# Performance work log

Measured on AMD Instinct MI355X. Metric: run time of the kernel, lower is better.

Reference implementation:

```python
import jax, jax.numpy as jnp
import numpy as np

NUM_Q_HEADS = 32
NUM_KV_HEADS = 8
HEAD_DIM = 128
ROPE_THETA = 10000.0
Q_SIZE = NUM_Q_HEADS * HEAD_DIM      # 4096
KV_SIZE = NUM_KV_HEADS * HEAD_DIM    # 1024


def _apply_rope_neox(x, positions, theta=ROPE_THETA):
    # x: [T, H, D]; neox-style rotate-halves RoPE
    T, H, D = x.shape
    half = D // 2
    inv_freq = 1.0 / (theta ** (jnp.arange(half, dtype=jnp.float32) / half))
    freqs = positions.astype(jnp.float32)[:, None] * inv_freq[None, :]  # [T, half]
    cos = jnp.cos(freqs)[:, None, :]  # [T, 1, half]
    sin = jnp.sin(freqs)[:, None, :]
    x1, x2 = x[..., :half], x[..., half:]
    return jnp.concatenate([x1 * cos - x2 * sin, x2 * cos + x1 * sin], axis=-1).astype(x.dtype)


def setup_inputs() -> dict:
    key = jax.random.key(0)
    k1, k2, k3 = jax.random.split(key, 3)
    T, E = 8192, 4096
    hidden_states = jax.random.normal(k1, (T, E), dtype=jnp.float32) * 0.02
    positions = jnp.arange(T, dtype=jnp.int32)
    w_qkv = jax.random.normal(k2, (E, Q_SIZE + 2 * KV_SIZE), dtype=jnp.float32) * 0.02
    w_o = jax.random.normal(k3, (Q_SIZE, E), dtype=jnp.float32) * 0.02
    return {"hidden_states": hidden_states, "positions": positions, "w_qkv": w_qkv, "w_o": w_o}


def reference(hidden_states, positions, w_qkv, w_o):
    T = hidden_states.shape[0]
    qkv = hidden_states @ w_qkv                              # [T, 6144]
    q = qkv[:, :Q_SIZE].reshape(T, NUM_Q_HEADS, HEAD_DIM)
    k = qkv[:, Q_SIZE:Q_SIZE + KV_SIZE].reshape(T, NUM_KV_HEADS, HEAD_DIM)
    v = qkv[:, Q_SIZE + KV_SIZE:]                            # [T, KV_SIZE] (unused by stub)
    q = _apply_rope_neox(q, positions)
    k = _apply_rope_neox(k, positions)
    # Attention is stubbed in the source (randn_like(q)); we use the RoPE'd q
    # as the deterministic stand-in so the pipeline stays reproducible.
    attn_output = q.reshape(T, Q_SIZE)
    output = attn_output @ w_o                               # [T, 4096]
    return output
```

## Files before the change

### kernel.cpp

```cpp
#include <hip/hip_runtime.h>
#include <hip/hip_bf16.h>
#include <stdint.h>

#define T_DIM 8192
#define E_DIM 4096
#define NQH   32
#define HD    128
#define QSZ   (NQH * HD)
#define QKV_COLS 6144

typedef unsigned short u16;
typedef __attribute__((ext_vector_type(8))) short   bf16x8;
typedef __attribute__((ext_vector_type(4))) float   f32x4;
typedef __attribute__((ext_vector_type(4))) unsigned short u16x4;

__device__ __forceinline__ u16 f2bf(float f) {
    uint32_t u = __float_as_uint(f);
    u += 0x7fffu + ((u >> 16) & 1u);
    return (u16)(u >> 16);
}
__device__ __forceinline__ float bf2f(u16 u) {
    return __uint_as_float(((uint32_t)u) << 16);
}

__device__ __forceinline__ void gload_lds16(u16* lds, const u16* g) {
    __builtin_amdgcn_global_load_lds(
        (const __attribute__((address_space(1))) uint32_t*)g,
        (__attribute__((address_space(3))) uint32_t*)lds,
        16, 0, 0);
}

__global__ void convert_f32_bf16(const float* __restrict__ in, u16* __restrict__ out, size_t n4) {
    size_t i = (size_t)blockIdx.x * blockDim.x + threadIdx.x;
    size_t stride = (size_t)gridDim.x * blockDim.x;
    for (; i < n4; i += stride) {
        float4 v = ((const float4*)in)[i];
        u16x4 o;
        o.x = f2bf(v.x); o.y = f2bf(v.y); o.z = f2bf(v.z); o.w = f2bf(v.w);
        ((u16x4*)out)[i] = o;
    }
}

__global__ void transpose_conv(const float* __restrict__ W, u16* __restrict__ Wt,
                               int K, int N, int ldW, int colOff) {
    __shared__ float tile[32][33];
    const int tx = threadIdx.x, ty = threadIdx.y;
    const int n0 = blockIdx.x * 32, k0 = blockIdx.y * 32;
#pragma unroll
    for (int j = 0; j < 4; ++j) {
        int k = k0 + ty + j * 8;
        tile[ty + j * 8][tx] = W[(size_t)k * ldW + colOff + n0 + tx];
    }
    __syncthreads();
#pragma unroll
    for (int j = 0; j < 4; ++j) {
        int n = n0 + ty + j * 8;
        Wt[(size_t)n * K + k0 + tx] = f2bf(tile[tx][ty + j * 8]);
    }
}

__global__ void rope_table(const int* __restrict__ pos, float2* __restrict__ tab) {
    int idx = blockIdx.x * blockDim.x + threadIdx.x;
    int t = idx >> 6, d = idx & 63;
    float inv = powf(10000.0f, -(float)d * (1.0f / 64.0f));
    float fr  = (float)pos[t] * inv;
    float s, c;
    sincosf(fr, &s, &c);
    tab[idx] = make_float2(c, s);
}

__device__ __forceinline__ void store_out(u16* p, float v)  { *p = f2bf(v); }
__device__ __forceinline__ void store_out(float* p, float v){ *p = v; }

#define BARS()    do { __builtin_amdgcn_sched_barrier(0); __builtin_amdgcn_s_barrier(); } while (0)
#define BARSPUB() do { __builtin_amdgcn_sched_barrier(0); __builtin_amdgcn_s_barrier(); \
                       __builtin_amdgcn_sched_barrier(0); } while (0)
#define VMC(N) asm volatile("s_waitcnt vmcnt(%0)" :: "n"(N) : "memory")

#define STG_A(buf, h, kOff) do { \
    const u16* s_ = sA + (size_t)(h) * 128 * K + (kOff); \
    u16* d_ = dL + (buf) * 32768 + (h) * 8192; \
    gload_lds16(d_, s_); gload_lds16(d_ + 4096, s_ + (size_t)64 * K); } while (0)
#define STG_B(buf, h, kOff) do { \
    const u16* s_ = sB + (size_t)(h) * 128 * K + (kOff); \
    u16* d_ = dL + 16384 + (buf) * 32768 + (h) * 8192; \
    gload_lds16(d_, s_); gload_lds16(d_ + 4096, s_ + (size_t)64 * K); } while (0)

#define RD_A(buf, miBase, d0, d1) do { _Pragma("unroll") \
    for (int m = 0; m < 4; ++m) { \
        const u16* p_ = lds + (buf) * 32768 + wm * 8192 + ((miBase) + m) * 1024 + aRow; \
        d0[m] = *(const bf16x8*)(p_ + cOf0); \
        d1[m] = *(const bf16x8*)(p_ + cOf1); } } while (0)
#define RD_B(buf, niBase, d0, d1) do { _Pragma("unroll") \
    for (int n = 0; n < 2; ++n) { \
        const int ni_ = (niBase) + n; \
        const u16* p_ = lds + (buf) * 32768 + 16384 + (ni_ >> 1) * 8192 + \
                        ((ni_ & 1) * 64 + wn * 16) * 64 + aRow; \
        d0[n] = *(const bf16x8*)(p_ + cOf0); \
        d1[n] = *(const bf16x8*)(p_ + cOf1); } } while (0)

#define MM(miBase, niBase, A0, A1, B0, B1) do { \
    __builtin_amdgcn_s_setprio(1); \
    _Pragma("unroll") for (int m = 0; m < 4; ++m) \
    _Pragma("unroll") for (int n = 0; n < 2; ++n) { \
        acc[(miBase) + m][(niBase) + n] = __builtin_amdgcn_mfma_f32_16x16x32_bf16( \
            A0[m], B0[n], acc[(miBase) + m][(niBase) + n], 0, 0, 0); \
        acc[(miBase) + m][(niBase) + n] = __builtin_amdgcn_mfma_f32_16x16x32_bf16( \
            A1[m], B1[n], acc[(miBase) + m][(niBase) + n], 0, 0, 0); } \
    __builtin_amdgcn_s_setprio(0); } while (0)

template <typename OutT, bool ROPE>
__global__ __launch_bounds__(512, 2) void gemm256(const u16* __restrict__ A,
                                                  const u16* __restrict__ Bt,
                                                  OutT* __restrict__ C,
                                                  const float2* __restrict__ tab,
                                                  int M, int N, int K) {
    __shared__ u16 lds[65536];
    const int tid  = threadIdx.x;
    const int lane = tid & 63;
    const int wid  = tid >> 6;
    const int wm = wid >> 2;
    const int wn = wid & 3;
    const int lr  = lane & 15;
    const int kq  = lane >> 4;
    const int lr7 = lr & 7;
    const int aRow = lr * 64;
    const int cOf0 = ((kq) ^ lr7) << 3;
    const int cOf1 = ((4 + kq) ^ lr7) << 3;

    const int nwg = gridDim.x;
    const int cpx = nwg >> 3;
    const int bid = blockIdx.x;
    const int swz = (bid & 7) * cpx + (bid >> 3);
    const int numM = M >> 8;
    const size_t rowBase = (size_t)(swz % numM) << 8;
    const size_t colBase = (size_t)(swz / numM) << 8;

    const int r0 = tid >> 3;
    const int cS = (((tid & 7) ^ (r0 & 7)) << 3);
    const u16* sA = A  + (rowBase + r0) * (size_t)K + cS;
    const u16* sB = Bt + (colBase + r0) * (size_t)K + cS;
    u16* dL = &lds[0] + tid * 8;

    f32x4 acc[8][4];
#pragma unroll
    for (int i = 0; i < 8; ++i)
#pragma unroll
        for (int j = 0; j < 4; ++j)
            acc[i][j] = (f32x4){0.f, 0.f, 0.f, 0.f};

    bf16x8 a0K0[4], a0K1[4], a4K0[4], a4K1[4];
    bf16x8 b01eK0[2], b01eK1[2], b01oK0[2], b01oK1[2], b23K0[2], b23K1[2];

    STG_A(0, 0, 0); STG_A(0, 1, 0); STG_B(0, 0, 0); STG_B(0, 1, 0);
    STG_B(1, 0, 64); STG_B(1, 1, 64);
    VMC(4);
    BARSPUB();
    RD_A(0, 0, a0K0, a0K1);
    RD_B(0, 0, b01eK0, b01eK1);

    const int nIter = K >> 7;
    for (int it = 0; it < nIter; ++it) {
        const int k1  = ((it << 1) + 1) << 6;
        const int kt2 = ((it << 1) + 2) << 6;
        const int kt3 = ((it << 1) + 3) << 6;
        const int k2c = (kt2 <= K - 64) ? kt2 : 0;
        const int k3c = (kt3 <= K - 64) ? kt3 : 0;

        STG_A(1, 0, k1);
        BARS();
        RD_B(0, 2, b23K0, b23K1);
        MM(0, 0, a0K0, a0K1, b01eK0, b01eK1);
        STG_A(1, 1, k1);
        BARS();
        RD_A(0, 4, a4K0, a4K1);
        MM(0, 2, a0K0, a0K1, b23K0, b23K1);
        STG_B(0, 0, k2c);
        BARS();
        MM(4, 2, a4K0, a4K1, b23K0, b23K1);
        STG_B(0, 1, k2c);
        VMC(4);
        BARSPUB();
        RD_A(1, 0, a0K0, a0K1);
        RD_B(1, 0, b01oK0, b01oK1);
        MM(4, 0, a4K0, a4K1, b01eK0, b01eK1);
        STG_A(0, 0, k2c);
        BARS();
        RD_B(1, 2, b23K0, b23K1);
        MM(0, 0, a0K0, a0K1, b01oK0, b01oK1);
        STG_A(0, 1, k2c);
        BARS();
        RD_A(1, 4, a4K0, a4K1);
        MM(0, 2, a0K0, a0K1, b23K0, b23K1);
        STG_B(1, 0, k3c);
        BARS();
        MM(4, 2, a4K0, a4K1, b23K0, b23K1);
        STG_B(1, 1, k3c);
        VMC(4);
        BARSPUB();
        RD_A(0, 0, a0K0, a0K1);
        RD_B(0, 0, b01eK0, b01eK1);
        MM(4, 0, a4K0, a4K1, b01oK0, b01oK1);
    }

    asm volatile("s_waitcnt vmcnt(0)" ::: "memory");

    if constexpr (ROPE) {
        const int dIdx = wn * 16 + lr;
#pragma unroll
        for (int mi = 0; mi < 8; ++mi)
#pragma unroll
            for (int r = 0; r < 4; ++r) {
                size_t row = rowBase + wm * 128 + mi * 16 + (kq << 2) + r;
                float2 cs = tab[row * 64 + dIdx];
#pragma unroll
                for (int hp = 0; hp < 2; ++hp) {
                    float x1 = acc[mi][hp * 2 + 0][r];
                    float x2 = acc[mi][hp * 2 + 1][r];
                    size_t c1 = colBase + hp * 128 + wn * 16 + lr;
                    C[row * (size_t)N + c1]      = f2bf(x1 * cs.x - x2 * cs.y);
                    C[row * (size_t)N + c1 + 64] = f2bf(x2 * cs.x + x1 * cs.y);
                }
            }
    } else {
#pragma unroll
        for (int mi = 0; mi < 8; ++mi)
#pragma unroll
            for (int ni = 0; ni < 4; ++ni)
#pragma unroll
                for (int r = 0; r < 4; ++r) {
                    size_t row = rowBase + wm * 128 + mi * 16 + (kq << 2) + r;
                    size_t col = colBase + ni * 64 + wn * 16 + lr;
                    store_out(&C[row * (size_t)N + col], acc[mi][ni][r]);
                }
    }
}

extern "C" void kernel_launch(void* const* d_in, const int* in_sizes, int n_in,
                              void* d_out, int out_size, void* d_ws, size_t ws_size,
                              hipStream_t stream) {
    const float* hidden    = (const float*)d_in[0];
    const int*   positions = (const int*)d_in[1];
    const float* w_qkv     = (const float*)d_in[2];
    const float* w_o       = (const float*)d_in[3];
    float* out = (float*)d_out;

    u16* Hb  = (u16*)d_ws;
    u16* WqT = Hb  + (size_t)T_DIM * E_DIM;
    u16* WoT = WqT + (size_t)QSZ * E_DIM;
    u16* Qb  = WoT + (size_t)E_DIM * QSZ;
    float2* tab = (float2*)WoT;

    convert_f32_bf16<<<2048, 256, 0, stream>>>(hidden, Hb, (size_t)T_DIM * E_DIM / 4);

    dim3 tb(32, 8);
    transpose_conv<<<dim3(QSZ / 32, E_DIM / 32), tb, 0, stream>>>(w_qkv, WqT, E_DIM, QSZ, QKV_COLS, 0);
    rope_table<<<(T_DIM * 64) / 256, 256, 0, stream>>>(positions, tab);

    gemm256<u16, true><<<dim3((T_DIM / 256) * (QSZ / 256)), 512, 0, stream>>>(
        Hb, WqT, Qb, tab, T_DIM, QSZ, E_DIM);

    transpose_conv<<<dim3(E_DIM / 32, QSZ / 32), tb, 0, stream>>>(w_o, WoT, QSZ, E_DIM, E_DIM, 0);

    gemm256<float, false><<<dim3((T_DIM / 256) * (E_DIM / 256)), 512, 0, stream>>>(
        Qb, WoT, out, nullptr, T_DIM, E_DIM, QSZ);
}
```

Measured before the change: 541.5 us.

## Restructure GEMM main loop into four-phase per-tile double-buffered schedule

Replaces the hand-interleaved two-tile software pipeline with a TILE macro. Each 64-wide K tile is processed in four phases, and each phase issues LDS reads and the next tile's global-to-LDS stage, then waits on lgkm/vm counters and a barrier before its MFMA block. The B fragment register sets are merged and the prologue stages only one tile ahead. This gives a simpler, more regular schedule, at the cost of roughly twice as many workgroup barriers per tile. It also adds explicit full LDS-read waits before each MFMA block, which may reduce overlap between memory traffic and matrix math.

```diff
diff --git a/kernel.cpp b/kernel.cpp
--- a/kernel.cpp
+++ b/kernel.cpp
@@ -72,10 +72,11 @@
 __device__ __forceinline__ void store_out(u16* p, float v)  { *p = f2bf(v); }
 __device__ __forceinline__ void store_out(float* p, float v){ *p = v; }
 
-#define BARS()    do { __builtin_amdgcn_sched_barrier(0); __builtin_amdgcn_s_barrier(); } while (0)
-#define BARSPUB() do { __builtin_amdgcn_sched_barrier(0); __builtin_amdgcn_s_barrier(); \
-                       __builtin_amdgcn_sched_barrier(0); } while (0)
-#define VMC(N) asm volatile("s_waitcnt vmcnt(%0)" :: "n"(N) : "memory")
+#define VMC(N)  asm volatile("s_waitcnt vmcnt(%0)"  :: "n"(N) : "memory")
+#define LGKM(N) asm volatile("s_waitcnt lgkmcnt(%0)" :: "n"(N) : "memory")
+#define PHASE_SYNC() do { __builtin_amdgcn_sched_barrier(0); __builtin_amdgcn_s_barrier(); \
+                          LGKM(0); __builtin_amdgcn_sched_barrier(0); } while (0)
+#define ENDBAR() do { __builtin_amdgcn_sched_barrier(0); __builtin_amdgcn_s_barrier(); } while (0)
 
 #define STG_A(buf, h, kOff) do { \
     const u16* s_ = sA + (size_t)(h) * 128 * K + (kOff); \
@@ -108,6 +109,36 @@
         acc[(miBase) + m][(niBase) + n] = __builtin_amdgcn_mfma_f32_16x16x32_bf16( \
             A1[m], B1[n], acc[(miBase) + m][(niBase) + n], 0, 0, 0); } \
     __builtin_amdgcn_s_setprio(0); } while (0)
+
+#define TILE(BUF, KN) do {                                                     \
+                                                                  \
+    RD_A(BUF, 0, a0K0, a0K1);                                                  \
+    RD_B(BUF, 0, b01K0, b01K1);                                                \
+    STG_A((BUF) ^ 1, 0, KN);                                                   \
+    LGKM(8);                                                                   \
+    PHASE_SYNC();                                                              \
+    MM(0, 0, a0K0, a0K1, b01K0, b01K1);                                        \
+    ENDBAR();                                                                  \
+                                                                  \
+    RD_A(BUF, 4, a4K0, a4K1);                                                  \
+    STG_A((BUF) ^ 1, 1, KN);                                                   \
+    VMC(4);                                                                    \
+    PHASE_SYNC();                                                              \
+    MM(4, 0, a4K0, a4K1, b01K0, b01K1);                                        \
+    ENDBAR();                                                                  \
+                                                                  \
+    RD_B(BUF, 2, b23K0, b23K1);                                                \
+    STG_B((BUF) ^ 1, 0, KN);                                                   \
+    PHASE_SYNC();                                                              \
+    MM(0, 2, a0K0, a0K1, b23K0, b23K1);                                        \
+    ENDBAR();                                                                  \
+                                                                  \
+    STG_B((BUF) ^ 1, 1, KN);                                                   \
+    VMC(2);                                                                    \
+    PHASE_SYNC();                                                              \
+    MM(4, 2, a4K0, a4K1, b23K0, b23K1);                                        \
+    ENDBAR();                                                                  \
+  } while (0)
 
 template <typename OutT, bool ROPE>
 __global__ __launch_bounds__(512, 2) void gemm256(const u16* __restrict__ A,
@@ -150,60 +181,23 @@
             acc[i][j] = (f32x4){0.f, 0.f, 0.f, 0.f};
 
     bf16x8 a0K0[4], a0K1[4], a4K0[4], a4K1[4];
-    bf16x8 b01eK0[2], b01eK1[2], b01oK0[2], b01oK1[2], b23K0[2], b23K1[2];
-
-    STG_A(0, 0, 0); STG_A(0, 1, 0); STG_B(0, 0, 0); STG_B(0, 1, 0);
-    STG_B(1, 0, 64); STG_B(1, 1, 64);
-    VMC(4);
-    BARSPUB();
-    RD_A(0, 0, a0K0, a0K1);
-    RD_B(0, 0, b01eK0, b01eK1);
-
-    const int nIter = K >> 7;
-    for (int it = 0; it < nIter; ++it) {
-        const int k1  = ((it << 1) + 1) << 6;
-        const int kt2 = ((it << 1) + 2) << 6;
-        const int kt3 = ((it << 1) + 3) << 6;
-        const int k2c = (kt2 <= K - 64) ? kt2 : 0;
-        const int k3c = (kt3 <= K - 64) ? kt3 : 0;
-
-        STG_A(1, 0, k1);
-        BARS();
-        RD_B(0, 2, b23K0, b23K1);
-        MM(0, 0, a0K0, a0K1, b01eK0, b01eK1);
-        STG_A(1, 1, k1);
-        BARS();
-        RD_A(0, 4, a4K0, a4K1);
-        MM(0, 2, a0K0, a0K1, b23K0, b23K1);
-        STG_B(0, 0, k2c);
-        BARS();
-        MM(4, 2, a4K0, a4K1, b23K0, b23K1);
-        STG_B(0, 1, k2c);
-        VMC(4);
-        BARSPUB();
-        RD_A(1, 0, a0K0, a0K1);
-        RD_B(1, 0, b01oK0, b01oK1);
-        MM(4, 0, a4K0, a4K1, b01eK0, b01eK1);
-        STG_A(0, 0, k2c);
-        BARS();
-        RD_B(1, 2, b23K0, b23K1);
-        MM(0, 0, a0K0, a0K1, b01oK0, b01oK1);
-        STG_A(0, 1, k2c);
-        BARS();
-        RD_A(1, 4, a4K0, a4K1);
-        MM(0, 2, a0K0, a0K1, b23K0, b23K1);
-        STG_B(1, 0, k3c);
-        BARS();
-        MM(4, 2, a4K0, a4K1, b23K0, b23K1);
-        STG_B(1, 1, k3c);
-        VMC(4);
-        BARSPUB();
-        RD_A(0, 0, a0K0, a0K1);
-        RD_B(0, 0, b01eK0, b01eK1);
-        MM(4, 0, a4K0, a4K1, b01oK0, b01oK1);
-    }
-
-    asm volatile("s_waitcnt vmcnt(0)" ::: "memory");
+    bf16x8 b01K0[2], b01K1[2], b23K0[2], b23K1[2];
+
+    STG_A(0, 0, 0); STG_A(0, 1, 0); STG_B(0, 0, 0);
+    STG_B(0, 1, 0);
+    VMC(2);
+    __builtin_amdgcn_sched_barrier(0);
+    __builtin_amdgcn_s_barrier();
+    __builtin_amdgcn_sched_barrier(0);
+
+    const int nT = K >> 6;
+    for (int t = 0; t < nT; t += 2) {
+        const int kN1 = (t + 1) << 6;
+        const int kN2 = (t + 2 < nT) ? ((t + 2) << 6) : 0;
+        TILE(0, kN1);
+        TILE(1, kN2);
+    }
+    VMC(0);
 
     if constexpr (ROPE) {
         const int dIdx = wn * 16 + lr;
```

Result: slower. 608.7 us (+12.4%).
